# Performance work log

Hardware: AMD Instinct MI355X
Metric: run time of the kernel (lower is better)

## Reference

```python
import jax, jax.numpy as jnp
import numpy as np

D_MODEL = 1024
N_HEADS = 16
D_K = D_MODEL // N_HEADS
D_FF = 4096
B, S = 2, 2048
EPS = 1e-5
SCALE = 0.02


def setup_inputs() -> dict:
    key = jax.random.key(0)
    ks = jax.random.split(key, 8)
    return {
        "x": jax.random.normal(ks[0], (B, S, D_MODEL), dtype=jnp.float32),
        "ln1_w": jnp.ones((D_MODEL,), jnp.float32),
        "ln1_b": jnp.zeros((D_MODEL,), jnp.float32),
        "Wq": jax.random.normal(ks[1], (D_MODEL, D_MODEL), jnp.float32) * SCALE,
        "bq": jnp.zeros((D_MODEL,), jnp.float32),
        "Wk": jax.random.normal(ks[2], (D_MODEL, D_MODEL), jnp.float32) * SCALE,
        "bk": jnp.zeros((D_MODEL,), jnp.float32),
        "Wv": jax.random.normal(ks[3], (D_MODEL, D_MODEL), jnp.float32) * SCALE,
        "bv": jnp.zeros((D_MODEL,), jnp.float32),
        "Wo": jax.random.normal(ks[4], (D_MODEL, D_MODEL), jnp.float32) * SCALE,
        "bo": jnp.zeros((D_MODEL,), jnp.float32),
        "ln2_w": jnp.ones((D_MODEL,), jnp.float32),
        "ln2_b": jnp.zeros((D_MODEL,), jnp.float32),
        "W1": jax.random.normal(ks[5], (D_MODEL, D_FF), jnp.float32) * SCALE,
        "b1": jnp.zeros((D_FF,), jnp.float32),
        "W2": jax.random.normal(ks[6], (D_FF, D_MODEL), jnp.float32) * SCALE,
        "b2": jnp.zeros((D_MODEL,), jnp.float32),
    }


def _layernorm(x, w, b):
    mu = jnp.mean(x, axis=-1, keepdims=True)
    var = jnp.mean(jnp.square(x - mu), axis=-1, keepdims=True)
    return (x - mu) * jax.lax.rsqrt(var + EPS) * w + b


def reference(x, ln1_w, ln1_b, Wq, bq, Wk, bk, Wv, bv, Wo, bo,
              ln2_w, ln2_b, W1, b1, W2, b2):
    # Pre-norm multi-head self-attention (dropout = identity, eval mode)
    h = _layernorm(x, ln1_w, ln1_b)                      # [B,S,D]
    q = (h @ Wq + bq).reshape(B, S, N_HEADS, D_K)        # [B,S,H,Dk]
    k = (h @ Wk + bk).reshape(B, S, N_HEADS, D_K)
    v = (h @ Wv + bv).reshape(B, S, N_HEADS, D_K)
    scores = jnp.einsum('bqhd,bkhd->bhqk', q, k) / jnp.sqrt(jnp.float32(D_K))
    attn = jax.nn.softmax(scores, axis=-1)               # [B,H,S,S]
    ctx = jnp.einsum('bhqk,bkhd->bqhd', attn, v).reshape(B, S, D_MODEL)
    x = x + (ctx @ Wo + bo)
    # Pre-norm FFN
    h2 = _layernorm(x, ln2_w, ln2_b)
    ff = jax.nn.relu(h2 @ W1 + b1) @ W2 + b2
    return x + ff
```

## Files before the change

kernel.cpp:

```cpp
#include <hip/hip_runtime.h>
#include <hip/hip_bf16.h>
#include <cstdint>
#include <cstddef>

typedef unsigned short ushort_t;
typedef __bf16 bf16x8 __attribute__((ext_vector_type(8)));
typedef float f32x4 __attribute__((ext_vector_type(4)));

#define D_MODEL 1024
#define D_FF 4096
#define BB 2
#define SS 2048
#define NH 16
#define MROWS (BB * SS)
#define KVBLK 64

__device__ __forceinline__ ushort_t f2bf(float f) {
  union { float f; unsigned u; } x; x.f = f;
  unsigned r = x.u + 0x7fffu + ((x.u >> 16) & 1u);
  return (ushort_t)(r >> 16);
}

__device__ __forceinline__ void gload_lds16(const void* g, void* l) {
  __builtin_amdgcn_global_load_lds((const __attribute__((address_space(1))) void*)g,
                                   (__attribute__((address_space(3))) void*)l, 16, 0, 0);
}

__device__ __forceinline__ float dpp_sum16(float x) {
  int v;
  v = __builtin_amdgcn_update_dpp(0, __float_as_int(x), 0xB1, 0xF, 0xF, true);
  x += __int_as_float(v);
  v = __builtin_amdgcn_update_dpp(0, __float_as_int(x), 0x4E, 0xF, 0xF, true);
  x += __int_as_float(v);
  v = __builtin_amdgcn_update_dpp(0, __float_as_int(x), 0x141, 0xF, 0xF, true);
  x += __int_as_float(v);
  v = __builtin_amdgcn_update_dpp(0, __float_as_int(x), 0x140, 0xF, 0xF, true);
  x += __int_as_float(v);
  return x;
}

__global__ __launch_bounds__(256) void ln_bf16_kernel(
    const float* __restrict__ x, const float* __restrict__ w,
    const float* __restrict__ b, ushort_t* __restrict__ out) {
  int row = blockIdx.x;
  int tid = threadIdx.x;
  int lane = tid & 63, wid = tid >> 6;
  const float4 v = ((const float4*)(x + (size_t)row * D_MODEL))[tid];
  float s = v.x + v.y + v.z + v.w;
  __shared__ float red[8];
  #pragma unroll
  for (int o = 32; o > 0; o >>= 1) s += __shfl_down(s, o);
  if (lane == 0) red[wid] = s;
  __syncthreads();
  float mu = (red[0] + red[1] + red[2] + red[3]) * (1.0f / D_MODEL);
  float d0 = v.x - mu, d1 = v.y - mu, d2 = v.z - mu, d3 = v.w - mu;
  float sq = d0 * d0 + d1 * d1 + d2 * d2 + d3 * d3;
  #pragma unroll
  for (int o = 32; o > 0; o >>= 1) sq += __shfl_down(sq, o);
  if (lane == 0) red[4 + wid] = sq;
  __syncthreads();
  float var = (red[4] + red[5] + red[6] + red[7]) * (1.0f / D_MODEL);
  float rstd = rsqrtf(var + 1e-5f);
  const float4 wv = ((const float4*)w)[tid];
  const float4 bv = ((const float4*)b)[tid];
  ushort4 o4;
  o4.x = f2bf(d0 * rstd * wv.x + bv.x);
  o4.y = f2bf(d1 * rstd * wv.y + bv.y);
  o4.z = f2bf(d2 * rstd * wv.z + bv.z);
  o4.w = f2bf(d3 * rstd * wv.w + bv.w);
  ((ushort4*)(out + (size_t)row * D_MODEL))[tid] = o4;
}

__global__ __launch_bounds__(256) void transpose_cast_kernel(
    const float* __restrict__ W, ushort_t* __restrict__ Wt, int K, int N) {
  __shared__ float tile[32][33];
  int bx = blockIdx.x * 32;
  int by = blockIdx.y * 32;
  int tx = threadIdx.x, ty = threadIdx.y;
  #pragma unroll
  for (int i = 0; i < 32; i += 8)
    tile[ty + i][tx] = W[(size_t)(by + ty + i) * N + bx + tx];
  __syncthreads();
  #pragma unroll
  for (int i = 0; i < 32; i += 8)
    Wt[(size_t)(bx + ty + i) * K + by + tx] = f2bf(tile[tx][ty + i]);
}

__global__ __launch_bounds__(256) void vtrans_kernel(
    const ushort_t* __restrict__ qkv, ushort_t* __restrict__ Vt) {
  __shared__ __align__(16) ushort_t T[64 * 64];
  const int tid = threadIdx.x;
  const int bh = blockIdx.y, b = bh >> 4, h = bh & 15;
  const int kv0 = blockIdx.x * 64;
  const ushort_t* Vp = qkv + (size_t)b * SS * 3072 + 2048 + h * 64;
  #pragma unroll
  for (int i = 0; i < 2; i++) {
    int idx = tid * 2 + i;
    int key = idx >> 3, c = idx & 7;
    bf16x8 v = *(const bf16x8*)(Vp + (size_t)(kv0 + key) * 3072 + c * 8);
    *(bf16x8*)(T + key * 64 + ((c ^ (key & 7)) * 8)) = v;
  }
  __syncthreads();
  int d = tid >> 2, kb = tid & 3;
  ushort_t o[16];
  #pragma unroll
  for (int j = 0; j < 16; j++) {
    int key = kb * 16 + j;
    o[j] = T[key * 64 + (((d >> 3) ^ (key & 7)) * 8) + (d & 7)];
  }
  ushort_t* dst = Vt + (size_t)(bh * 64 + d) * SS + kv0 + kb * 16;
  *(bf16x8*)dst = *(bf16x8*)&o[0];
  *(bf16x8*)(dst + 8) = *(bf16x8*)&o[8];
}

template <int EPI>
__global__ __launch_bounds__(512, 2) void gemm256_kernel(
    const ushort_t* __restrict__ A, const ushort_t* __restrict__ Bt,
    const float* __restrict__ bias, void* __restrict__ Cout,
    int M, int N, int K, int NTn, int MTN, int Ksplit) {
  __shared__ __align__(16) ushort_t lds[4][2][8192];
  const int tid = threadIdx.x, lane = tid & 63, wid = tid >> 6;
  const int wm = wid >> 2, wn = wid & 3;
  const int rl = lane & 15, cg = lane >> 4;
  int nwg = gridDim.x;
  int q = nwg >> 3, rr = nwg & 7;
  int xcd = blockIdx.x & 7, idx = blockIdx.x >> 3;
  int wgid = (xcd < rr ? xcd * (q + 1) : rr * (q + 1) + (xcd - rr) * q) + idx;
  const int s = wgid / MTN;
  int rem = wgid - s * MTN;
  const int row0 = (rem / NTn) * 256, col0 = (rem - (rem / NTn) * NTn) * 256;
  const int k0 = s * Ksplit;
  const int NT = Ksplit / 32;

  f32x4 acc[8][4] = {};

  auto stage = [&](int t) {
    int b = t & 3;
    int kk = k0 + t * 32;
    #pragma unroll
    for (int i = 0; i < 2; i++) {
      int P = (wid * 2 + i) * 1024 + lane * 16;
      int L = P ^ (((P >> 7) & 7) << 4);
      int row = L >> 6, kc = (L >> 4) & 3;
      gload_lds16(A + (size_t)(row0 + row) * K + kk + kc * 8,
                  &lds[b][0][(wid * 2 + i) * 512]);
      gload_lds16(Bt + (size_t)(col0 + row) * K + kk + kc * 8,
                  &lds[b][1][(wid * 2 + i) * 512]);
    }
  };

  auto compute = [&](int t) {
    int b = t & 3;
    bf16x8 af[8], bfv[4];
    #pragma unroll
    for (int mi = 0; mi < 8; mi++) {
      int r = wm * 128 + mi * 16 + rl;
      int L = r * 64 + cg * 16;
      int P = L ^ (((L >> 7) & 7) << 4);
      af[mi] = *(const bf16x8*)&lds[b][0][P >> 1];
    }
    #pragma unroll
    for (int ni = 0; ni < 4; ni++) {
      int r = wn * 64 + ni * 16 + rl;
      int L = r * 64 + cg * 16;
      int P = L ^ (((L >> 7) & 7) << 4);
      bfv[ni] = *(const bf16x8*)&lds[b][1][P >> 1];
    }
    __builtin_amdgcn_s_setprio(1);
    #pragma unroll
    for (int mi = 0; mi < 8; mi++)
      #pragma unroll
      for (int ni = 0; ni < 4; ni++)
        acc[mi][ni] = __builtin_amdgcn_mfma_f32_16x16x32_bf16(af[mi], bfv[ni], acc[mi][ni], 0, 0, 0);
    __builtin_amdgcn_s_setprio(0);
  };

  stage(0); stage(1); stage(2);
  for (int t = 0; t < NT; ++t) {
    if (t < NT - 2)       asm volatile("s_waitcnt vmcnt(8)" ::: "memory");
    else if (t == NT - 2) asm volatile("s_waitcnt vmcnt(4)" ::: "memory");
    else                  asm volatile("s_waitcnt vmcnt(0)" ::: "memory");
    __builtin_amdgcn_s_barrier();
    __builtin_amdgcn_sched_barrier(0);
    if (t + 3 < NT) stage(t + 3);
    compute(t);
  }

  if (EPI == 2) {
    float* out = (float*)Cout + (size_t)s * M * N;
    #pragma unroll
    for (int ni = 0; ni < 4; ni++) {
      int col = col0 + wn * 64 + ni * 16 + rl;
      #pragma unroll
      for (int mi = 0; mi < 8; mi++) {
        int rowb = row0 + wm * 128 + mi * 16 + cg * 4;
        #pragma unroll
        for (int j = 0; j < 4; j++)
          out[(size_t)(rowb + j) * N + col] = acc[mi][ni][j];
      }
    }
  } else {
    ushort_t* out = (ushort_t*)Cout;
    #pragma unroll
    for (int ni = 0; ni < 4; ni++) {
      int col = col0 + wn * 64 + ni * 16 + rl;
      float bv = bias[col];
      float sc = (EPI == 0 && col < 1024) ? 0.18033688011f : 1.0f;
      #pragma unroll
      for (int mi = 0; mi < 8; mi++) {
        int rowb = row0 + wm * 128 + mi * 16 + cg * 4;
        #pragma unroll
        for (int j = 0; j < 4; j++) {
          float v = acc[mi][ni][j] + bv;
          if (EPI == 1) v = fmaxf(v, 0.0f);
          if (EPI == 0) v *= sc;
          out[(size_t)(rowb + j) * N + col] = f2bf(v);
        }
      }
    }
  }
}

__global__ __launch_bounds__(256) void reduce_kernel(
    const float* __restrict__ p, const float* __restrict__ bias,
    const float* __restrict__ resid, float* __restrict__ out,
    int S, size_t total4, size_t stride4) {
  const float4* p4 = (const float4*)p;
  const float4* r4 = (const float4*)resid;
  const float4* b4 = (const float4*)bias;
  float4* o4 = (float4*)out;
  for (size_t i = (size_t)blockIdx.x * 256 + threadIdx.x; i < total4;
       i += (size_t)gridDim.x * 256) {
    float4 a = r4[i];
    float4 bb = b4[i & 255];
    a.x += bb.x; a.y += bb.y; a.z += bb.z; a.w += bb.w;
    for (int s = 0; s < S; ++s) {
      float4 v = p4[(size_t)s * stride4 + i];
      a.x += v.x; a.y += v.y; a.z += v.z; a.w += v.w;
    }
    o4[i] = a;
  }
}

__global__ __launch_bounds__(256) void attn_kernel(
    const ushort_t* __restrict__ qkv, const ushort_t* __restrict__ Vt,
    ushort_t* __restrict__ ctx) {
  __shared__ __align__(16) ushort_t Kl[2][64 * 64];
  __shared__ __align__(16) ushort_t Vl[2][64 * 64];
  __shared__ __align__(16) ushort_t Pl[4][16 * 64];
  const int tid = threadIdx.x, lane = tid & 63, wid = tid >> 6;
  int bid = blockIdx.y * 32 + blockIdx.x;
  int w = (bid & 7) * 128 + (bid >> 3);
  const int bh = w >> 5, qt = w & 31;
  const int b = bh >> 4, h = bh & 15;
  const int q0 = qt * 64 + wid * 16;
  const ushort_t* Qp = qkv + (size_t)b * SS * 3072 + h * 64;
  const ushort_t* Kp = Qp + 1024;
  const ushort_t* Vg = Vt + (size_t)bh * 64 * SS;

  bf16x8 qf[2];
  {
    int qr = q0 + (lane & 15);
    #pragma unroll
    for (int s2 = 0; s2 < 2; s2++)
      qf[s2] = *(const bf16x8*)(Qp + (size_t)qr * 3072 + s2 * 32 + (lane >> 4) * 8);
  }
  float l[4];
  f32x4 acc[4] = {};
  #pragma unroll
  for (int r = 0; r < 4; r++) l[r] = 0.f;

  const int NT = SS / KVBLK;

  auto stageK = [&](int buf, int t) {
    int kv = t * KVBLK;
    #pragma unroll
    for (int i = 0; i < 2; i++) {
      int base = wid * 128 + i * 64;
      int idx = base + lane;
      int R = idx >> 3, c = idx & 7;
      int key = (R & 15) * 4 + (R >> 4);
      gload_lds16(Kp + (size_t)(kv + key) * 3072 + ((c ^ (R & 7)) * 8),
                  &Kl[buf][base * 8]);
    }
  };
  auto stageV = [&](int buf, int t) {
    int kv = t * KVBLK;
    #pragma unroll
    for (int i = 0; i < 2; i++) {
      int base = wid * 128 + i * 64;
      int idx = base + lane;
      int d = idx >> 3, c = idx & 7;
      gload_lds16(Vg + (size_t)d * SS + kv + ((c ^ (d & 7)) * 8),
                  &Vl[buf][base * 8]);
    }
  };

  stageK(0, 0);
  stageV(0, 0);
  int cur = 0;
  for (int t = 0; t < NT; ++t) {
    __syncthreads();
    if (t + 1 < NT) { stageK(cur ^ 1, t + 1); stageV(cur ^ 1, t + 1); }

    f32x4 s4[4] = {};
    #pragma unroll
    for (int g = 0; g < 4; g++) {
      const ushort_t* kr = &Kl[cur][(g * 16 + (lane & 15)) * 64];
      bf16x8 kf0 = *(const bf16x8*)(kr + (((lane >> 4)) ^ ((lane & 15) & 7)) * 8);
      bf16x8 kf1 = *(const bf16x8*)(kr + ((4 + (lane >> 4)) ^ ((lane & 15) & 7)) * 8);
      s4[g] = __builtin_amdgcn_mfma_f32_16x16x32_bf16(qf[0], kf0, s4[g], 0, 0, 0);
      s4[g] = __builtin_amdgcn_mfma_f32_16x16x32_bf16(qf[1], kf1, s4[g], 0, 0, 0);
    }
    const int qrow = (lane >> 4) * 4;
    const int cp = (lane & 15) >> 1, hf = (lane & 15) & 1;
    #pragma unroll
    for (int r = 0; r < 4; r++) {
      float p0 = __builtin_amdgcn_exp2f(s4[0][r]);
      float p1 = __builtin_amdgcn_exp2f(s4[1][r]);
      float p2 = __builtin_amdgcn_exp2f(s4[2][r]);
      float p3 = __builtin_amdgcn_exp2f(s4[3][r]);
      l[r] += (p0 + p1) + (p2 + p3);
      unsigned w0, w1;
      asm("v_cvt_pk_bf16_f32 %0, %1, %2" : "=v"(w0) : "v"(p0), "v"(p1));
      asm("v_cvt_pk_bf16_f32 %0, %1, %2" : "=v"(w1) : "v"(p2), "v"(p3));
      uint2 pw; pw.x = w0; pw.y = w1;
      int qq = qrow + r;
      *(uint2*)(&Pl[wid][qq * 64 + ((cp ^ (qq & 7)) * 8) + hf * 4]) = pw;
    }
    asm volatile("s_waitcnt lgkmcnt(0)" ::: "memory");
    __builtin_amdgcn_sched_barrier(0);
    bf16x8 pf[2];
    {
      int qq = lane & 15;
      #pragma unroll
      for (int ks = 0; ks < 2; ks++) {
        int c = ks * 4 + (lane >> 4);
        pf[ks] = *(const bf16x8*)(&Pl[wid][qq * 64 + ((c ^ (qq & 7)) * 8)]);
      }
    }
    #pragma unroll
    for (int f = 0; f < 4; f++) {
      int d = f * 16 + (lane & 15);
      #pragma unroll
      for (int ks = 0; ks < 2; ks++) {
        int chunk = (ks * 4 + (lane >> 4)) ^ (d & 7);
        bf16x8 vf = *(const bf16x8*)(&Vl[cur][d * 64 + chunk * 8]);
        acc[f] = __builtin_amdgcn_mfma_f32_16x16x32_bf16(pf[ks], vf, acc[f], 0, 0, 0);
      }
    }
    cur ^= 1;
  }

  #pragma unroll
  for (int r = 0; r < 4; r++) l[r] = dpp_sum16(l[r]);
  float rl4[4];
  #pragma unroll
  for (int r = 0; r < 4; r++) rl4[r] = 1.0f / l[r];
  #pragma unroll
  for (int f = 0; f < 4; f++)
    #pragma unroll
    for (int r = 0; r < 4; r++) {
      int row = b * SS + q0 + (lane >> 4) * 4 + r;
      int col = h * 64 + f * 16 + (lane & 15);
      ctx[(size_t)row * D_MODEL + col] = f2bf(acc[f][r] * rl4[r]);
    }
}

extern "C" void kernel_launch(void* const* d_in, const int* in_sizes, int n_in,
                              void* d_out, int out_size, void* d_ws, size_t ws_size,
                              hipStream_t stream) {
  const float* x    = (const float*)d_in[0];
  const float* ln1w = (const float*)d_in[1];
  const float* ln1b = (const float*)d_in[2];
  const float* Wq   = (const float*)d_in[3];
  const float* bq   = (const float*)d_in[4];
  const float* Wk   = (const float*)d_in[5];
  const float* bk   = (const float*)d_in[6];
  const float* Wv   = (const float*)d_in[7];
  const float* bv   = (const float*)d_in[8];
  const float* Wo   = (const float*)d_in[9];
  const float* bo   = (const float*)d_in[10];
  const float* ln2w = (const float*)d_in[11];
  const float* ln2b = (const float*)d_in[12];
  const float* W1   = (const float*)d_in[13];
  const float* b1   = (const float*)d_in[14];
  const float* W2   = (const float*)d_in[15];
  const float* b2   = (const float*)d_in[16];

  char* ws = (char*)d_ws;
  size_t off = 0;
  auto alloc = [&](size_t bytes) {
    void* p = ws + off;
    off += (bytes + 255) & ~(size_t)255;
    return p;
  };
  ushort_t* Wt_qkv = (ushort_t*)alloc((size_t)3072 * 1024 * 2);
  ushort_t* Wt_o   = (ushort_t*)alloc((size_t)1024 * 1024 * 2);
  ushort_t* Wt_1   = (ushort_t*)alloc((size_t)4096 * 1024 * 2);
  ushort_t* Wt_2   = (ushort_t*)alloc((size_t)1024 * 4096 * 2);
  float*    bqkv   = (float*)alloc((size_t)3072 * 4);
  ushort_t* qkvb   = (ushort_t*)alloc((size_t)MROWS * 3072 * 2);
  ushort_t* ctxb   = (ushort_t*)alloc((size_t)MROWS * 1024 * 2);
  ushort_t* hbuf   = (ushort_t*)alloc((size_t)MROWS * 1024 * 2);
  float*    x2     = (float*)alloc((size_t)MROWS * 1024 * 4);
  ushort_t* Vtb    = (ushort_t*)alloc((size_t)BB * NH * 64 * SS * 2);
  ushort_t* ff1    = qkvb;
  float*    outp   = (float*)d_out;

  const size_t partial1 = (size_t)MROWS * 1024 * 4;
  int S = 1;
  if (ws_size - off >= 4 * partial1 + 256) S = 4;
  else if (ws_size - off >= 2 * partial1 + 256) S = 2;
  float* pbuf = (float*)alloc((size_t)S * partial1);

  dim3 tb(32, 8);
  transpose_cast_kernel<<<dim3(32, 32), tb, 0, stream>>>(Wq, Wt_qkv, 1024, 1024);
  transpose_cast_kernel<<<dim3(32, 32), tb, 0, stream>>>(Wk, Wt_qkv + 1024 * 1024, 1024, 1024);
  transpose_cast_kernel<<<dim3(32, 32), tb, 0, stream>>>(Wv, Wt_qkv + 2 * 1024 * 1024, 1024, 1024);
  transpose_cast_kernel<<<dim3(32, 32), tb, 0, stream>>>(Wo, Wt_o, 1024, 1024);
  transpose_cast_kernel<<<dim3(128, 32), tb, 0, stream>>>(W1, Wt_1, 1024, 4096);
  transpose_cast_kernel<<<dim3(32, 128), tb, 0, stream>>>(W2, Wt_2, 4096, 1024);
  hipMemcpyAsync(bqkv,        bq, 1024 * 4, hipMemcpyDeviceToDevice, stream);
  hipMemcpyAsync(bqkv + 1024, bk, 1024 * 4, hipMemcpyDeviceToDevice, stream);
  hipMemcpyAsync(bqkv + 2048, bv, 1024 * 4, hipMemcpyDeviceToDevice, stream);

  ln_bf16_kernel<<<MROWS, 256, 0, stream>>>(x, ln1w, ln1b, hbuf);
  gemm256_kernel<0><<<dim3(16 * 12), 512, 0, stream>>>(
      hbuf, Wt_qkv, bqkv, qkvb, MROWS, 3072, 1024, 12, 16 * 12, 1024);
  vtrans_kernel<<<dim3(SS / 64, BB * NH), 256, 0, stream>>>(qkvb, Vtb);
  attn_kernel<<<dim3(SS / 64, BB * NH), 256, 0, stream>>>(qkvb, Vtb, ctxb);
  gemm256_kernel<2><<<dim3(16 * 4 * S), 512, 0, stream>>>(
      ctxb, Wt_o, nullptr, pbuf, MROWS, 1024, 1024, 4, 16 * 4, 1024 / S);
  reduce_kernel<<<2048, 256, 0, stream>>>(pbuf, bo, x, x2, S,
      (size_t)MROWS * 1024 / 4, (size_t)MROWS * 1024 / 4);
  ln_bf16_kernel<<<MROWS, 256, 0, stream>>>(x2, ln2w, ln2b, hbuf);
  gemm256_kernel<1><<<dim3(16 * 16), 512, 0, stream>>>(
      hbuf, Wt_1, b1, ff1, MROWS, D_FF, 1024, 16, 16 * 16, 1024);
  gemm256_kernel<2><<<dim3(16 * 4 * S), 512, 0, stream>>>(
      ff1, Wt_2, nullptr, pbuf, MROWS, 1024, 4096, 4, 16 * 4, 4096 / S);
  reduce_kernel<<<2048, 256, 0, stream>>>(pbuf, b2, x2, outp, S,
      (size_t)MROWS * 1024 / 4, (size_t)MROWS * 1024 / 4);
}
```

Before: 274.1 us.

## Switch GEMMs to 128x128 tiles, drop split-K reduce, fuse bias+residual epilogue

Replaces the 256x256 tile, 512-thread GEMM with a 128x128 tile, 256-thread variant. This gives more workgroups per launch, so the split-K partial buffers and separate reduce kernels are no longer needed, and bias and residual are added directly in the output-projection and FFN2 epilogues. Staging addresses are precomputed once in both GEMM and attention, and the attention K/V staging is merged with a loop unrolled by two to drop the buffer toggle. Smaller tiles lower data reuse per workgroup and raise operand traffic from global memory and LDS.

```diff
diff --git a/kernel.cpp b/kernel.cpp
--- a/kernel.cpp
+++ b/kernel.cpp
@@ -114,47 +114,50 @@
 }
 
 template <int EPI>
-__global__ __launch_bounds__(512, 2) void gemm256_kernel(
+__global__ __launch_bounds__(256, 2) void gemm128_kernel(
     const ushort_t* __restrict__ A, const ushort_t* __restrict__ Bt,
-    const float* __restrict__ bias, void* __restrict__ Cout,
-    int M, int N, int K, int NTn, int MTN, int Ksplit) {
-  __shared__ __align__(16) ushort_t lds[4][2][8192];
+    const float* __restrict__ bias, const float* __restrict__ resid,
+    void* __restrict__ Cout, int M, int N, int K, int NTn) {
+  __shared__ __align__(16) ushort_t lds[4][2][4096];
   const int tid = threadIdx.x, lane = tid & 63, wid = tid >> 6;
-  const int wm = wid >> 2, wn = wid & 3;
+  const int wm = wid >> 1, wn = wid & 1;
   const int rl = lane & 15, cg = lane >> 4;
   int nwg = gridDim.x;
   int q = nwg >> 3, rr = nwg & 7;
   int xcd = blockIdx.x & 7, idx = blockIdx.x >> 3;
   int wgid = (xcd < rr ? xcd * (q + 1) : rr * (q + 1) + (xcd - rr) * q) + idx;
-  const int s = wgid / MTN;
-  int rem = wgid - s * MTN;
-  const int row0 = (rem / NTn) * 256, col0 = (rem - (rem / NTn) * NTn) * 256;
-  const int k0 = s * Ksplit;
-  const int NT = Ksplit / 32;
-
-  f32x4 acc[8][4] = {};
+  const int row0 = (wgid / NTn) * 128, col0 = (wgid - (wgid / NTn) * NTn) * 128;
+  const int NT = K / 32;
+
+  int soff[2], ldso[2];
+  #pragma unroll
+  for (int i = 0; i < 2; i++) {
+    int ci = wid * 128 + i * 64 + lane;
+    int P = ci * 16;
+    int L = P ^ (((P >> 7) & 7) << 4);
+    int row = L >> 6, kc = (L >> 4) & 3;
+    soff[i] = row * K + kc * 8;
+    ldso[i] = (wid * 128 + i * 64) * 8;
+  }
+
+  f32x4 acc[4][4] = {};
 
   auto stage = [&](int t) {
     int b = t & 3;
-    int kk = k0 + t * 32;
+    int kk = t * 32;
     #pragma unroll
     for (int i = 0; i < 2; i++) {
-      int P = (wid * 2 + i) * 1024 + lane * 16;
-      int L = P ^ (((P >> 7) & 7) << 4);
-      int row = L >> 6, kc = (L >> 4) & 3;
-      gload_lds16(A + (size_t)(row0 + row) * K + kk + kc * 8,
-                  &lds[b][0][(wid * 2 + i) * 512]);
-      gload_lds16(Bt + (size_t)(col0 + row) * K + kk + kc * 8,
-                  &lds[b][1][(wid * 2 + i) * 512]);
+      gload_lds16(A + (size_t)row0 * K + kk + soff[i], &lds[b][0][ldso[i]]);
+      gload_lds16(Bt + (size_t)col0 * K + kk + soff[i], &lds[b][1][ldso[i]]);
     }
   };
 
   auto compute = [&](int t) {
     int b = t & 3;
-    bf16x8 af[8], bfv[4];
-    #pragma unroll
-    for (int mi = 0; mi < 8; mi++) {
-      int r = wm * 128 + mi * 16 + rl;
+    bf16x8 af[4], bfv[4];
+    #pragma unroll
+    for (int mi = 0; mi < 4; mi++) {
+      int r = wm * 64 + mi * 16 + rl;
       int L = r * 64 + cg * 16;
       int P = L ^ (((L >> 7) & 7) << 4);
       af[mi] = *(const bf16x8*)&lds[b][0][P >> 1];
@@ -168,7 +171,7 @@
     }
     __builtin_amdgcn_s_setprio(1);
     #pragma unroll
-    for (int mi = 0; mi < 8; mi++)
+    for (int mi = 0; mi < 4; mi++)
       #pragma unroll
       for (int ni = 0; ni < 4; ni++)
         acc[mi][ni] = __builtin_amdgcn_mfma_f32_16x16x32_bf16(af[mi], bfv[ni], acc[mi][ni], 0, 0, 0);
@@ -187,16 +190,18 @@
   }
 
   if (EPI == 2) {
-    float* out = (float*)Cout + (size_t)s * M * N;
+    float* out = (float*)Cout;
     #pragma unroll
     for (int ni = 0; ni < 4; ni++) {
       int col = col0 + wn * 64 + ni * 16 + rl;
+      float bv = bias[col];
       #pragma unroll
-      for (int mi = 0; mi < 8; mi++) {
-        int rowb = row0 + wm * 128 + mi * 16 + cg * 4;
+      for (int mi = 0; mi < 4; mi++) {
+        int rowb = row0 + wm * 64 + mi * 16 + cg * 4;
         #pragma unroll
         for (int j = 0; j < 4; j++)
-          out[(size_t)(rowb + j) * N + col] = acc[mi][ni][j];
+          out[(size_t)(rowb + j) * N + col] =
+              acc[mi][ni][j] + bv + resid[(size_t)(rowb + j) * N + col];
       }
     }
   } else {
@@ -207,8 +212,8 @@
       float bv = bias[col];
       float sc = (EPI == 0 && col < 1024) ? 0.18033688011f : 1.0f;
       #pragma unroll
-      for (int mi = 0; mi < 8; mi++) {
-        int rowb = row0 + wm * 128 + mi * 16 + cg * 4;
+      for (int mi = 0; mi < 4; mi++) {
+        int rowb = row0 + wm * 64 + mi * 16 + cg * 4;
         #pragma unroll
         for (int j = 0; j < 4; j++) {
           float v = acc[mi][ni][j] + bv;
@@ -218,27 +223,6 @@
         }
       }
     }
-  }
-}
-
-__global__ __launch_bounds__(256) void reduce_kernel(
-    const float* __restrict__ p, const float* __restrict__ bias,
-    const float* __restrict__ resid, float* __restrict__ out,
-    int S, size_t total4, size_t stride4) {
-  const float4* p4 = (const float4*)p;
-  const float4* r4 = (const float4*)resid;
-  const float4* b4 = (const float4*)bias;
-  float4* o4 = (float4*)out;
-  for (size_t i = (size_t)blockIdx.x * 256 + threadIdx.x; i < total4;
-       i += (size_t)gridDim.x * 256) {
-    float4 a = r4[i];
-    float4 bb = b4[i & 255];
-    a.x += bb.x; a.y += bb.y; a.z += bb.z; a.w += bb.w;
-    for (int s = 0; s < S; ++s) {
-      float4 v = p4[(size_t)s * stride4 + i];
-      a.x += v.x; a.y += v.y; a.z += v.z; a.w += v.w;
-    }
-    o4[i] = a;
   }
 }
 
@@ -272,41 +256,34 @@
 
   const int NT = SS / KVBLK;
 
-  auto stageK = [&](int buf, int t) {
-    int kv = t * KVBLK;
-    #pragma unroll
-    for (int i = 0; i < 2; i++) {
-      int base = wid * 128 + i * 64;
-      int idx = base + lane;
-      int R = idx >> 3, c = idx & 7;
-      int key = (R & 15) * 4 + (R >> 4);
-      gload_lds16(Kp + (size_t)(kv + key) * 3072 + ((c ^ (R & 7)) * 8),
-                  &Kl[buf][base * 8]);
-    }
+  int ksrc[2], vsrc[2];
+  #pragma unroll
+  for (int i = 0; i < 2; i++) {
+    int idx = wid * 128 + i * 64 + lane;
+    int R = idx >> 3, c = idx & 7;
+    int key = (R & 15) * 4 + (R >> 4);
+    ksrc[i] = key * 3072 + ((c ^ (R & 7)) * 8);
+    vsrc[i] = R * SS + ((c ^ (R & 7)) * 8);
+  }
+  const int ldsb = wid * 1024;
+
+  auto stageKV = [&](int buf, int t) {
+    size_t kvK = (size_t)t * KVBLK * 3072;
+    int kvV = t * KVBLK;
+    gload_lds16(Kp + kvK + ksrc[0], &Kl[buf][ldsb]);
+    gload_lds16(Kp + kvK + ksrc[1], &Kl[buf][ldsb + 512]);
+    gload_lds16(Vg + kvV + vsrc[0], &Vl[buf][ldsb]);
+    gload_lds16(Vg + kvV + vsrc[1], &Vl[buf][ldsb + 512]);
   };
-  auto stageV = [&](int buf, int t) {
-    int kv = t * KVBLK;
-    #pragma unroll
-    for (int i = 0; i < 2; i++) {
-      int base = wid * 128 + i * 64;
-      int idx = base + lane;
-      int d = idx >> 3, c = idx & 7;
-      gload_lds16(Vg + (size_t)d * SS + kv + ((c ^ (d & 7)) * 8),
-                  &Vl[buf][base * 8]);
-    }
-  };
-
-  stageK(0, 0);
-  stageV(0, 0);
-  int cur = 0;
-  for (int t = 0; t < NT; ++t) {
+
+  auto body = [&](int t, int cb) {
     __syncthreads();
-    if (t + 1 < NT) { stageK(cur ^ 1, t + 1); stageV(cur ^ 1, t + 1); }
+    if (t + 1 < NT) stageKV(cb ^ 1, t + 1);
 
     f32x4 s4[4] = {};
     #pragma unroll
     for (int g = 0; g < 4; g++) {
-      const ushort_t* kr = &Kl[cur][(g * 16 + (lane & 15)) * 64];
+      const ushort_t* kr = &Kl[cb][(g * 16 + (lane & 15)) * 64];
       bf16x8 kf0 = *(const bf16x8*)(kr + (((lane >> 4)) ^ ((lane & 15) & 7)) * 8);
       bf16x8 kf1 = *(const bf16x8*)(kr + ((4 + (lane >> 4)) ^ ((lane & 15) & 7)) * 8);
       s4[g] = __builtin_amdgcn_mfma_f32_16x16x32_bf16(qf[0], kf0, s4[g], 0, 0, 0);
@@ -345,11 +322,16 @@
       #pragma unroll
       for (int ks = 0; ks < 2; ks++) {
         int chunk = (ks * 4 + (lane >> 4)) ^ (d & 7);
-        bf16x8 vf = *(const bf16x8*)(&Vl[cur][d * 64 + chunk * 8]);
+        bf16x8 vf = *(const bf16x8*)(&Vl[cb][d * 64 + chunk * 8]);
         acc[f] = __builtin_amdgcn_mfma_f32_16x16x32_bf16(pf[ks], vf, acc[f], 0, 0, 0);
       }
     }
-    cur ^= 1;
+  };
+
+  stageKV(0, 0);
+  for (int t = 0; t < NT; t += 2) {
+    body(t, 0);
+    body(t + 1, 1);
   }
 
   #pragma unroll
@@ -408,12 +390,6 @@
   ushort_t* ff1    = qkvb;
   float*    outp   = (float*)d_out;
 
-  const size_t partial1 = (size_t)MROWS * 1024 * 4;
-  int S = 1;
-  if (ws_size - off >= 4 * partial1 + 256) S = 4;
-  else if (ws_size - off >= 2 * partial1 + 256) S = 2;
-  float* pbuf = (float*)alloc((size_t)S * partial1);
-
   dim3 tb(32, 8);
   transpose_cast_kernel<<<dim3(32, 32), tb, 0, stream>>>(Wq, Wt_qkv, 1024, 1024);
   transpose_cast_kernel<<<dim3(32, 32), tb, 0, stream>>>(Wk, Wt_qkv + 1024 * 1024, 1024, 1024);
@@ -426,19 +402,15 @@
   hipMemcpyAsync(bqkv + 2048, bv, 1024 * 4, hipMemcpyDeviceToDevice, stream);
 
   ln_bf16_kernel<<<MROWS, 256, 0, stream>>>(x, ln1w, ln1b, hbuf);
-  gemm256_kernel<0><<<dim3(16 * 12), 512, 0, stream>>>(
-      hbuf, Wt_qkv, bqkv, qkvb, MROWS, 3072, 1024, 12, 16 * 12, 1024);
+  gemm128_kernel<0><<<dim3(24 * 32), 256, 0, stream>>>(
+      hbuf, Wt_qkv, bqkv, nullptr, qkvb, MROWS, 3072, 1024, 24);
   vtrans_kernel<<<dim3(SS / 64, BB * NH), 256, 0, stream>>>(qkvb, Vtb);
   attn_kernel<<<dim3(SS / 64, BB * NH), 256, 0, stream>>>(qkvb, Vtb, ctxb);
-  gemm256_kernel<2><<<dim3(16 * 4 * S), 512, 0, stream>>>(
-      ctxb, Wt_o, nullptr, pbuf, MROWS, 1024, 1024, 4, 16 * 4, 1024 / S);
-  reduce_kernel<<<2048, 256, 0, stream>>>(pbuf, bo, x, x2, S,
-      (size_t)MROWS * 1024 / 4, (size_t)MROWS * 1024 / 4);
+  gemm128_kernel<2><<<dim3(8 * 32), 256, 0, stream>>>(
+      ctxb, Wt_o, bo, x, x2, MROWS, 1024, 1024, 8);
   ln_bf16_kernel<<<MROWS, 256, 0, stream>>>(x2, ln2w, ln2b, hbuf);
-  gemm256_kernel<1><<<dim3(16 * 16), 512, 0, stream>>>(
-      hbuf, Wt_1, b1, ff1, MROWS, D_FF, 1024, 16, 16 * 16, 1024);
-  gemm256_kernel<2><<<dim3(16 * 4 * S), 512, 0, stream>>>(
-      ff1, Wt_2, nullptr, pbuf, MROWS, 1024, 4096, 4, 16 * 4, 4096 / S);
-  reduce_kernel<<<2048, 256, 0, stream>>>(pbuf, b2, x2, outp, S,
-      (size_t)MROWS * 1024 / 4, (size_t)MROWS * 1024 / 4);
-}
+  gemm128_kernel<1><<<dim3(32 * 32), 256, 0, stream>>>(
+      hbuf, Wt_1, b1, nullptr, ff1, MROWS, D_FF, 1024, 32);
+  gemm128_kernel<2><<<dim3(8 * 32), 256, 0, stream>>>(
+      ff1, Wt_2, b2, x2, outp, MROWS, 1024, 4096, 8);
+}
```

Result: faster. 254.6 us (-7.1%).
